# Optimization experiments

Hardware: AMD Instinct MI355X
Metric: run time of the kernel (lower is better)

The kernel has to match this reference:

```python
import jax, jax.numpy as jnp
import numpy as np

N_NODES = 50000
N_FEAT = 63          # nodeChannels C = N_FEAT + 1 = 64
N_EDGES = 800000
N_LABELS = 10000
BATCH = 4
N_LAYERS = 5
C = N_FEAT + 1


def setup_inputs() -> dict:
    key = jax.random.key(0)
    ks = jax.random.split(key, 16)
    s = 0.05  # small init scale for numerical sanity
    return {
        "cov": jax.random.normal(ks[0], (BATCH, N_LABELS), jnp.float32),
        "nodes": jax.random.normal(ks[1], (N_NODES, N_FEAT), jnp.float32),
        "edges": jax.random.randint(ks[2], (2, N_EDGES), 0, N_NODES, jnp.int64 if jax.config.jax_enable_x64 else jnp.int32),
        "count2label": jnp.arange(N_LABELS, dtype=jnp.int32),
        "ggc_weight": jax.random.normal(ks[3], (N_LAYERS, C, C), jnp.float32) * s,
        "gru_w_ih": jax.random.normal(ks[4], (3 * C, C), jnp.float32) * s,
        "gru_w_hh": jax.random.normal(ks[5], (3 * C, C), jnp.float32) * s,
        "gru_b_ih": jax.random.normal(ks[6], (3 * C,), jnp.float32) * s,
        "gru_b_hh": jax.random.normal(ks[7], (3 * C,), jnp.float32) * s,
        "ai_w": jax.random.normal(ks[8], (2 * C, 2 * C), jnp.float32) * s,
        "ai_b": jax.random.normal(ks[9], (2 * C,), jnp.float32) * s,
        "aj_w": jax.random.normal(ks[10], (2 * C, 2 * C), jnp.float32) * s,
        "aj_b": jax.random.normal(ks[11], (2 * C,), jnp.float32) * s,
        "mlp_w": jax.random.normal(ks[12], (256, 2 * C), jnp.float32) * s,
        "mlp_b": jax.random.normal(ks[13], (256,), jnp.float32) * s,
        "critic_w": jax.random.normal(ks[14], (1, 256), jnp.float32) * s,
        "critic_b": jax.random.normal(ks[15], (1,), jnp.float32) * s,
    }


def _gru_cell(m, h, w_ih, w_hh, b_ih, b_hh):
    # torch GRUCell, gate order r, z, n
    gx = m @ w_ih.T + b_ih   # [..., 3C]
    gh = h @ w_hh.T + b_hh
    c = h.shape[-1]
    xr, xz, xn = gx[..., :c], gx[..., c:2 * c], gx[..., 2 * c:]
    hr, hz, hn = gh[..., :c], gh[..., c:2 * c], gh[..., 2 * c:]
    r = jax.nn.sigmoid(xr + hr)
    z = jax.nn.sigmoid(xz + hz)
    n = jnp.tanh(xn + r * hn)
    return (1.0 - z) * n + z * h


def reference(cov, nodes, edges, count2label, ggc_weight,
              gru_w_ih, gru_w_hh, gru_b_ih, gru_b_hh,
              ai_w, ai_b, aj_w, aj_b, mlp_w, mlp_b, critic_w, critic_b):
    n, f = nodes.shape
    b = cov.shape[0]
    # scatter coverage into per-graph node channel: covInGraph[count2label] = cov
    cov_in_graph = jnp.zeros((b, n), cov.dtype).at[:, count2label].set(cov)
    # batched node input [B, N, C]; batched graph = B identical copies w/ offset edges
    x0 = jnp.concatenate(
        [jnp.broadcast_to(nodes, (b, n, f)), cov_in_graph[..., None]], axis=-1)
    src, dst = edges[0], edges[1]

    def scatter_add(mb):  # [N, C] -> [N, C]: sum messages from source at target
        return jax.ops.segment_sum(mb[src], dst, num_segments=n)

    x = x0
    for i in range(ggc_weight.shape[0]):
        m = x @ ggc_weight[i]                     # dense per-layer matmul [B,N,C]
        agg = jax.vmap(scatter_add)(m)            # edge scatter-add propagate
        x = _gru_cell(agg, x, gru_w_ih, gru_w_hh, gru_b_ih, gru_b_hh)

    # attention gate: sigmoid(Wi cat) * relu(Wj cat), cat = [x, x0]
    cat = jnp.concatenate([x, x0], axis=-1)       # [B, N, 2C]
    att = jax.nn.sigmoid(cat @ ai_w.T + ai_b) * jax.nn.relu(cat @ aj_w.T + aj_b)
    pooled = jax.nn.relu(att.sum(axis=1))         # global_add_pool -> [B, 2C]
    state = jax.nn.relu(pooled @ mlp_w.T + mlp_b) # graphmlp
    return state @ critic_w.T + critic_b          # critic value [B, 1]
```

## Files before the change

### kernel.cpp

```cpp
#include <hip/hip_runtime.h>
#include <math.h>

#define NN 50000
#define NF 63
#define NE 800000
#define NL 10000
#define NB 4
#define NLAY 5
#define BN (NB*NN)
#define NTILES (BN/64)
#define SCAN_NBLK ((NN+255)/256)
#define HIST_NBLK ((NE+255)/256)
#define X0_NBLK ((BN*16)/256)
#define COV_NBLK ((NB*NL+255)/256)

using f32x4  = __attribute__((ext_vector_type(4))) float;
using f32x2  = __attribute__((ext_vector_type(2))) float;
using bf16x8 = __attribute__((ext_vector_type(8))) __bf16;

__device__ __forceinline__ float frcp(float x){ return __builtin_amdgcn_rcpf(x); }
__device__ __forceinline__ float sigm(float v){ return frcp(1.f + __expf(-v)); }
__device__ __forceinline__ float tanh_f(float v){ return fmaf(-2.f, frcp(__expf(2.f*v) + 1.f), 1.f); }

__device__ __forceinline__ ushort f2bf(float f){
    uint u = __builtin_bit_cast(uint, f);
    u += 0x7fffu + ((u >> 16) & 1u);
    return (ushort)(u >> 16);
}
__device__ __forceinline__ float bf_lo(uint v){ return __builtin_bit_cast(float, v << 16); }
__device__ __forceinline__ float bfu(ushort v){ return __builtin_bit_cast(float, ((uint)v) << 16); }

__device__ __forceinline__ uchar f2fp8(float v){
    int enc = __builtin_amdgcn_cvt_pk_fp8_f32(v, v, 0, false);
    return (uchar)(enc & 0xff);
}

__device__ __forceinline__ bf16x8 ldfrag(const ushort* p){
    uint4 v = *(const uint4*)p;
    return __builtin_bit_cast(bf16x8, v);
}
__device__ __forceinline__ f32x4 MFMA(bf16x8 a, bf16x8 b, f32x4 c){
    return __builtin_amdgcn_mfma_f32_16x16x32_bf16(a, b, c, 0, 0, 0);
}

__global__ void k_setup(const int* __restrict__ edges, int* __restrict__ cnt,
                        const float* __restrict__ wih, const float* __restrict__ whh,
                        const float* __restrict__ aiw, const float* __restrict__ ajw,
                        const float* __restrict__ ggc,
                        ushort* __restrict__ whhb, ushort* __restrict__ aiwb,
                        ushort* __restrict__ ajwb, ushort* __restrict__ wfb,
                        const float* __restrict__ nodes, ushort* __restrict__ x0I,
                        uchar* __restrict__ x0F){
    int bid = blockIdx.x;
    if (bid < HIST_NBLK){
        int e = bid*256 + threadIdx.x;
        if (e < NE) atomicAdd(&cnt[edges[NE + e]], 1);
        return;
    }
    if (bid < HIST_NBLK + 416){
        int i = (bid - HIST_NBLK)*256 + threadIdx.x;
        if (i < 12288)        whhb[i]        = f2bf(whh[i]);
        else if (i < 28672)   aiwb[i-12288]  = f2bf(aiw[i-12288]);
        else if (i < 45056)   ajwb[i-28672]  = f2bf(ajw[i-28672]);
        else if (i < 106496){
            int t = i - 45056;
            int lay = t / 12288;
            int rem = t % 12288;
            int n = rem >> 6, k = rem & 63;
            const float* W  = ggc + lay*4096 + k*64;
            const float* wr = wih + n*64;
            float s = 0.f;
            #pragma unroll 8
            for (int c = 0; c < 64; ++c) s = fmaf(W[c], wr[c], s);
            wfb[t] = f2bf(s);
        }
        return;
    }
    int f = (bid - HIST_NBLK - 416)*256 + threadIdx.x;
    int row = f >> 4, c4 = f & 15;
    int n = row % NN, b = row / NN;
    float v[4];
    #pragma unroll
    for (int i = 0; i < 4; ++i){
        int c = c4*4 + i;
        v[i] = (c < NF) ? nodes[(size_t)n*NF + c] : 0.f;
    }
    uint2 pk;
    pk.x = (uint)f2bf(v[0]) | ((uint)f2bf(v[1]) << 16);
    pk.y = (uint)f2bf(v[2]) | ((uint)f2bf(v[3]) << 16);
    *(uint2*)(x0I + ((size_t)n*4 + b)*64 + c4*4) = pk;
    if (b == 0){
        uint q = 0;
        q = (uint)__builtin_amdgcn_cvt_pk_fp8_f32(v[0], v[1], (int)q, false);
        q = (uint)__builtin_amdgcn_cvt_pk_fp8_f32(v[2], v[3], (int)q, true);
        *(uint*)(x0F + (size_t)n*64 + c4*4) = q;
    }
}

__global__ void k_scan1(const int* __restrict__ cnt, int* __restrict__ tmp, int* __restrict__ bsum,
                        const float* __restrict__ cov, const int* __restrict__ c2l,
                        ushort* __restrict__ x0I, ushort* __restrict__ covB){
    if (blockIdx.x >= SCAN_NBLK){
        int i = (blockIdx.x - SCAN_NBLK)*256 + threadIdx.x;
        if (i < NB*NL){
            int b = i / NL, j = i % NL;
            int nd = c2l[j];
            ushort vb = f2bf(cov[i]);
            x0I[((size_t)nd*4 + b)*64 + 63] = vb;
            covB[(size_t)nd*4 + b] = vb;
        }
        return;
    }
    __shared__ int sh[256];
    int tx = threadIdx.x, i = blockIdx.x*256 + tx;
    int v = (i < NN) ? cnt[i] : 0;
    sh[tx] = v; __syncthreads();
    for (int off = 1; off < 256; off <<= 1){
        int u = (tx >= off) ? sh[tx-off] : 0;
        __syncthreads();
        sh[tx] += u;
        __syncthreads();
    }
    int incl = sh[tx];
    if (i < NN) tmp[i] = incl - v;
    if (tx == 255) bsum[blockIdx.x] = incl;
}

__global__ void k_scan3(const int* __restrict__ tmp, const int* __restrict__ bsum,
                        int* __restrict__ row_start, int* __restrict__ cursor){
    __shared__ int sh[256];
    int tx = threadIdx.x;
    int v = (tx < SCAN_NBLK) ? bsum[tx] : 0;
    sh[tx] = v; __syncthreads();
    for (int off = 1; off < 256; off <<= 1){
        int u = (tx >= off) ? sh[tx-off] : 0;
        __syncthreads();
        sh[tx] += u;
        __syncthreads();
    }
    int boff = sh[blockIdx.x] - bsum[blockIdx.x];
    int i = blockIdx.x*256 + tx;
    if (i < NN){
        int rs = tmp[i] + boff;
        row_start[i] = rs;
        cursor[i] = rs;
    }
    if (i == 0) row_start[NN] = NE;
}

__global__ void k_fillcsr(const int* __restrict__ edges, int* __restrict__ cursor, int* __restrict__ csr_src){
    int e = blockIdx.x*256 + threadIdx.x;
    if (e < NE){
        int d = edges[NE + e];
        int pos = atomicAdd(&cursor[d], 1);
        csr_src[pos] = edges[e];
    }
}

__device__ __forceinline__ void gather0q(const uchar* __restrict__ x0F,
                                         const ushort* __restrict__ covB,
                                         const int* __restrict__ csr_src,
                                         int e0, int e1, int l,
                                         ushort* __restrict__ sAgg, int rbase){
    const int qn = l >> 4, t = l & 15;
    const uint off = (uint)(t*4);
    f32x2 a01 = (f32x2){0.f,0.f}, a23 = (f32x2){0.f,0.f};
    float c = 0.f;
    int e = e0;
    for (; e + 16 <= e1; e += 16){
        int s[16];
        #pragma unroll
        for (int j = 0; j < 16; ++j) s[j] = csr_src[e + j];
        uint v[16];
        #pragma unroll
        for (int j = 0; j < 16; ++j) v[j] = *(const uint*)(x0F + (size_t)s[j]*64 + off);
        #pragma unroll
        for (int j = 0; j < 16; ++j){
            a01 += __builtin_amdgcn_cvt_pk_f32_fp8(v[j], false);
            a23 += __builtin_amdgcn_cvt_pk_f32_fp8(v[j], true);
        }
        if (t < 4){
            #pragma unroll
            for (int j = 0; j < 16; ++j) c += bf_lo((uint)covB[(size_t)s[j]*4 + t]);
        }
    }
    if (e < e1){
        int s[16];
        #pragma unroll
        for (int j = 0; j < 16; ++j){ int ee = e + j; if (ee >= e1) ee = e1 - 1; s[j] = csr_src[ee]; }
        uint v[16];
        #pragma unroll
        for (int j = 0; j < 16; ++j){
            v[j] = *(const uint*)(x0F + (size_t)s[j]*64 + off);
            if (e + j >= e1) v[j] = 0u;
        }
        #pragma unroll
        for (int j = 0; j < 16; ++j){
            a01 += __builtin_amdgcn_cvt_pk_f32_fp8(v[j], false);
            a23 += __builtin_amdgcn_cvt_pk_f32_fp8(v[j], true);
        }
        if (t < 4){
            #pragma unroll
            for (int j = 0; j < 16; ++j){
                float cv = bf_lo((uint)covB[(size_t)s[j]*4 + t]);
                c += (e + j < e1) ? cv : 0.f;
            }
        }
    }
    uint2 pk;
    pk.x = (uint)f2bf(a01.x) | ((uint)f2bf(a01.y) << 16);
    pk.y = (uint)f2bf(a23.x) | ((uint)f2bf(a23.y) << 16);
    #pragma unroll
    for (int b = 0; b < 4; ++b){
        float cb = __shfl(c, (l & 48) | b);
        uint2 o = pk;
        if (t == 15) o.y = (o.y & 0xffffu) | ((uint)f2bf(cb) << 16);
        *(uint2*)(&sAgg[(size_t)(rbase + qn*4 + b)*72 + t*4]) = o;
    }
}

__device__ __forceinline__ void load8(uint4 v[8], const uchar* __restrict__ xF,
                                      const int* __restrict__ csr_src,
                                      int eb, int e1, uint off){
    #pragma unroll
    for (int j = 0; j < 8; ++j){
        int ee = eb + j; if (ee >= e1) ee = e1 - 1;
        int s = csr_src[ee];
        v[j] = *(const uint4*)(xF + (size_t)s*256 + off);
    }
}
__device__ __forceinline__ void conv8(const uint4 v[8], int eb, int e1, f32x2 ac[8]){
    #pragma unroll
    for (int j = 0; j < 8; ++j){
        uint4 x = v[j];
        if (eb + j >= e1) x = (uint4){0u,0u,0u,0u};
        ac[0] += __builtin_amdgcn_cvt_pk_f32_fp8(x.x, false);
        ac[1] += __builtin_amdgcn_cvt_pk_f32_fp8(x.x, true);
        ac[2] += __builtin_amdgcn_cvt_pk_f32_fp8(x.y, false);
        ac[3] += __builtin_amdgcn_cvt_pk_f32_fp8(x.y, true);
        ac[4] += __builtin_amdgcn_cvt_pk_f32_fp8(x.z, false);
        ac[5] += __builtin_amdgcn_cvt_pk_f32_fp8(x.z, true);
        ac[6] += __builtin_amdgcn_cvt_pk_f32_fp8(x.w, false);
        ac[7] += __builtin_amdgcn_cvt_pk_f32_fp8(x.w, true);
    }
}

__device__ __forceinline__ void gather4q(const uchar* __restrict__ xF,
                                         const int* __restrict__ csr_src,
                                         int e0, int e1, int l,
                                         ushort* __restrict__ sAgg, int rbase){
    const int qn = l >> 4;
    const int t  = l & 15;
    const uint off = (uint)(t*16);
    f32x2 ac[8];
    #pragma unroll
    for (int k = 0; k < 8; ++k) ac[k] = (f32x2){0.f,0.f};

    uint4 va[8], vb[8];
    int eb = e0;
    if (eb < e1){
        load8(va, xF, csr_src, eb, e1, off);
        while (true){
            int ebB = eb + 8;
            if (ebB >= e1){ conv8(va, eb, e1, ac); break; }
            load8(vb, xF, csr_src, ebB, e1, off);
            conv8(va, eb, e1, ac);
            int ebA = ebB + 8;
            if (ebA >= e1){ conv8(vb, ebB, e1, ac); break; }
            load8(va, xF, csr_src, ebA, e1, off);
            conv8(vb, ebB, e1, ac);
            eb = ebA;
        }
    }

    const int row = rbase + qn*4 + (t >> 2);
    const int c0  = (t & 3)*16;
    uint4 o0, o1;
    o0.x = (uint)f2bf(ac[0].x) | ((uint)f2bf(ac[0].y) << 16);
    o0.y = (uint)f2bf(ac[1].x) | ((uint)f2bf(ac[1].y) << 16);
    o0.z = (uint)f2bf(ac[2].x) | ((uint)f2bf(ac[2].y) << 16);
    o0.w = (uint)f2bf(ac[3].x) | ((uint)f2bf(ac[3].y) << 16);
    o1.x = (uint)f2bf(ac[4].x) | ((uint)f2bf(ac[4].y) << 16);
    o1.y = (uint)f2bf(ac[5].x) | ((uint)f2bf(ac[5].y) << 16);
    o1.z = (uint)f2bf(ac[6].x) | ((uint)f2bf(ac[6].y) << 16);
    o1.w = (uint)f2bf(ac[7].x) | ((uint)f2bf(ac[7].y) << 16);
    *(uint4*)(&sAgg[(size_t)row*72 + c0])     = o0;
    *(uint4*)(&sAgg[(size_t)row*72 + c0 + 8]) = o1;
}

__device__ __forceinline__ void gru_core(const ushort* sAgg, const ushort* sX,
                                         const ushort* __restrict__ wfb, const ushort* __restrict__ whhb,
                                         const float* __restrict__ bih, const float* __restrict__ bhh,
                                         int li, int q, int n0, float xv[4][4]){
    f32x4 Cr[4], Cz[4], Cxn[4], Chn[4];
    #pragma unroll
    for (int m = 0; m < 4; ++m){
        Cr[m]=(f32x4){0.f,0.f,0.f,0.f}; Cz[m]=(f32x4){0.f,0.f,0.f,0.f};
        Cxn[m]=(f32x4){0.f,0.f,0.f,0.f}; Chn[m]=(f32x4){0.f,0.f,0.f,0.f};
    }
    __builtin_amdgcn_s_setprio(1);
    #pragma unroll
    for (int ks = 0; ks < 4; ++ks){
        const ushort* wb = (ks < 2) ? wfb : whhb;
        const ushort* sT = (ks < 2) ? sAgg : sX;
        const int kb = (ks & 1)*32;
        bf16x8 Br = ldfrag(wb + (size_t)(n0 + li)*64 + kb + q*8);
        bf16x8 Bz = ldfrag(wb + (size_t)(64 + n0 + li)*64 + kb + q*8);
        bf16x8 Bn = ldfrag(wb + (size_t)(128 + n0 + li)*64 + kb + q*8);
        #pragma unroll
        for (int m = 0; m < 4; ++m){
            bf16x8 A = ldfrag(&sT[(m*16 + li)*72 + kb + q*8]);
            Cr[m] = MFMA(A, Br, Cr[m]);
            Cz[m] = MFMA(A, Bz, Cz[m]);
            if (ks < 2) Cxn[m] = MFMA(A, Bn, Cxn[m]);
            else        Chn[m] = MFMA(A, Bn, Chn[m]);
        }
    }
    __builtin_amdgcn_s_setprio(0);
    const int c = n0 + li;
    const float br_ = bih[c]     + bhh[c];
    const float bz_ = bih[64+c]  + bhh[64+c];
    const float bn_ = bih[128+c];
    const float bh_ = bhh[128+c];
    #pragma unroll
    for (int m = 0; m < 4; ++m){
        #pragma unroll
        for (int rg = 0; rg < 4; ++rg){
            int rl = m*16 + q*4 + rg;
            float r = sigm(Cr[m][rg] + br_);
            float z = sigm(Cz[m][rg] + bz_);
            float nng = tanh_f(Cxn[m][rg] + bn_ + r*(Chn[m][rg] + bh_));
            xv[m][rg] = (1.f - z)*nng + z*bfu(sX[rl*72 + c]);
        }
    }
}

__device__ __forceinline__ void store_state(ushort* sAgg, uchar* sF8, int tx, int w, int li, int q,
                                            const float xv[4][4], int R0,
                                            ushort* __restrict__ xout, uchar* __restrict__ xFout){
    __syncthreads();
    const int c = 16*w + li;
    #pragma unroll
    for (int m = 0; m < 4; ++m)
        #pragma unroll
        for (int rg = 0; rg < 4; ++rg){
            int r = m*16 + q*4 + rg;
            sAgg[r*72 + c] = f2bf(xv[m][rg]);
            sF8[r*64 + c]  = f2fp8(xv[m][rg]);
        }
    __syncthreads();
    #pragma unroll
    for (int it = 0; it < 2; ++it){
        int idx = it*256 + tx, r = idx >> 3, g = idx & 7;
        *(uint4*)(xout + (size_t)(R0 + r)*64 + g*8) = *(const uint4*)(&sAgg[r*72 + g*8]);
    }
    {
        int r = tx >> 2, g = tx & 3;
        *(uint4*)(xFout + (size_t)(R0 + r)*64 + g*16) = *(const uint4*)(&sF8[r*64 + g*16]);
    }
}

__global__ __launch_bounds__(256, 4) void k_gru0f(const uchar* __restrict__ x0F,
                                               const ushort* __restrict__ covB,
                                               const int* __restrict__ row_start,
                                               const int* __restrict__ csr_src,
                                               const ushort* __restrict__ x0I,
                                               const ushort* __restrict__ wfb, const ushort* __restrict__ whhb,
                                               const float* __restrict__ bih, const float* __restrict__ bhh,
                                               ushort* __restrict__ xout, uchar* __restrict__ xFout){
    __shared__ __align__(16) ushort sAgg[64*72];
    __shared__ __align__(16) ushort sX[64*72];
    __shared__ __align__(16) uchar  sF8[64*64];
    const int tx = threadIdx.x;
    const int l  = tx & 63, li = l & 15, q = l >> 4;
    const int w  = __builtin_amdgcn_readfirstlane(tx >> 6);
    const int R0 = blockIdx.x*64;
    const int d  = blockIdx.x*16 + w*4 + (l >> 4);
    const int e0 = row_start[d], e1 = row_start[d+1];

    #pragma unroll
    for (int it = 0; it < 2; ++it){
        int idx = it*256 + tx, r = idx >> 3, g = idx & 7;
        *(uint4*)(&sX[r*72 + g*8]) = *(const uint4*)(x0I + (size_t)(R0 + r)*64 + g*8);
    }
    gather0q(x0F, covB, csr_src, e0, e1, l, sAgg, w*16);
    __syncthreads();

    float xv[4][4];
    gru_core(sAgg, sX, wfb, whhb, bih, bhh, li, q, 16*w, xv);
    store_state(sAgg, sF8, tx, w, li, q, xv, R0, xout, xFout);
}

__global__ __launch_bounds__(256, 4) void k_gruFf(const uchar* __restrict__ xFin,
                                               const int* __restrict__ row_start,
                                               const int* __restrict__ csr_src,
                                               const ushort* __restrict__ xsrc,
                                               const ushort* __restrict__ wfb, const ushort* __restrict__ whhb,
                                               const float* __restrict__ bih, const float* __restrict__ bhh,
                                               ushort* __restrict__ xout, uchar* __restrict__ xFout){
    __shared__ __align__(16) ushort sAgg[64*72];
    __shared__ __align__(16) ushort sX[64*72];
    __shared__ __align__(16) uchar  sF8[64*64];
    const int tx = threadIdx.x;
    const int l  = tx & 63, li = l & 15, q = l >> 4;
    const int w  = __builtin_amdgcn_readfirstlane(tx >> 6);
    const int R0 = blockIdx.x*64;
    const int d  = blockIdx.x*16 + w*4 + (l >> 4);
    const int e0 = row_start[d], e1 = row_start[d+1];

    #pragma unroll
    for (int it = 0; it < 2; ++it){
        int idx = it*256 + tx, r = idx >> 3, g = idx & 7;
        *(uint4*)(&sX[r*72 + g*8]) = *(const uint4*)(xsrc + (size_t)(R0 + r)*64 + g*8);
    }
    gather4q(xFin, csr_src, e0, e1, l, sAgg, w*16);
    __syncthreads();

    float xv[4][4];
    gru_core(sAgg, sX, wfb, whhb, bih, bhh, li, q, 16*w, xv);
    store_state(sAgg, sF8, tx, w, li, q, xv, R0, xout, xFout);
}

__global__ __launch_bounds__(256, 4) void k_gruLf(const uchar* __restrict__ xFin,
                                               const int* __restrict__ row_start,
                                               const int* __restrict__ csr_src,
                                               const ushort* __restrict__ xsrc,
                                               const ushort* __restrict__ wfb, const ushort* __restrict__ whhb,
                                               const float* __restrict__ bih, const float* __restrict__ bhh,
                                               const ushort* __restrict__ x0I,
                                               const ushort* __restrict__ aiwb, const float* __restrict__ aib,
                                               const ushort* __restrict__ ajwb, const float* __restrict__ ajb,
                                               float* __restrict__ pooled16){
    __shared__ __align__(16) ushort sAgg[64*72];
    __shared__ __align__(16) ushort sX[64*72];
    const int tx = threadIdx.x;
    const int l  = tx & 63, li = l & 15, q = l >> 4;
    const int w  = __builtin_amdgcn_readfirstlane(tx >> 6);
    const int R0 = blockIdx.x*64;
    const int d  = blockIdx.x*16 + w*4 + (l >> 4);
    const int e0 = row_start[d], e1 = row_start[d+1];

    #pragma unroll
    for (int it = 0; it < 2; ++it){
        int idx = it*256 + tx, r = idx >> 3, g = idx & 7;
        *(uint4*)(&sX[r*72 + g*8]) = *(const uint4*)(xsrc + (size_t)(R0 + r)*64 + g*8);
    }
    gather4q(xFin, csr_src, e0, e1, l, sAgg, w*16);
    __syncthreads();

    float xv[4][4];
    gru_core(sAgg, sX, wfb, whhb, bih, bhh, li, q, 16*w, xv);
    __syncthreads();

    const int c = 16*w + li;
    #pragma unroll
    for (int m = 0; m < 4; ++m)
        #pragma unroll
        for (int rg = 0; rg < 4; ++rg)
            sAgg[(m*16 + q*4 + rg)*72 + c] = f2bf(xv[m][rg]);
    #pragma unroll
    for (int it = 0; it < 2; ++it){
        int idx = it*256 + tx, r = idx >> 3, g = idx & 7;
        *(uint4*)(&sX[r*72 + g*8]) = *(const uint4*)(x0I + (size_t)(R0 + r)*64 + g*8);
    }
    __syncthreads();

    f32x4 Ai[2][4], Aj[2][4];
    #pragma unroll
    for (int t = 0; t < 2; ++t)
        #pragma unroll
        for (int m = 0; m < 4; ++m){ Ai[t][m]=(f32x4){0.f,0.f,0.f,0.f}; Aj[t][m]=(f32x4){0.f,0.f,0.f,0.f}; }

    const int nb0 = 32*w;
    __builtin_amdgcn_s_setprio(1);
    #pragma unroll
    for (int ks = 0; ks < 4; ++ks){
        const ushort* sT = (ks < 2) ? sAgg : sX;
        const int kb = (ks & 1)*32;
        bf16x8 Bi[2], Bj[2];
        #pragma unroll
        for (int t = 0; t < 2; ++t){
            Bi[t] = ldfrag(aiwb + (size_t)(nb0 + 16*t + li)*128 + ks*32 + q*8);
            Bj[t] = ldfrag(ajwb + (size_t)(nb0 + 16*t + li)*128 + ks*32 + q*8);
        }
        #pragma unroll
        for (int m = 0; m < 4; ++m){
            bf16x8 A = ldfrag(&sT[(m*16 + li)*72 + kb + q*8]);
            #pragma unroll
            for (int t = 0; t < 2; ++t){
                Ai[t][m] = MFMA(A, Bi[t], Ai[t][m]);
                Aj[t][m] = MFMA(A, Bj[t], Aj[t][m]);
            }
        }
    }
    __builtin_amdgcn_s_setprio(0);

    float* pb = pooled16 + (size_t)(blockIdx.x & 15)*512;
    #pragma unroll
    for (int t = 0; t < 2; ++t){
        int cc = nb0 + 16*t + li;
        float bia = aib[cc], bja = ajb[cc];
        float vs[4] = {0.f, 0.f, 0.f, 0.f};
        #pragma unroll
        for (int m = 0; m < 4; ++m){
            #pragma unroll
            for (int rg = 0; rg < 4; ++rg){
                float s = sigm(Ai[t][m][rg] + bia);
                float a = Aj[t][m][rg] + bja;
                a = a > 0.f ? a : 0.f;
                vs[rg] += s*a;
            }
        }
        #pragma unroll
        for (int b = 0; b < 4; ++b){
            vs[b] += __shfl_xor(vs[b], 16);
            vs[b] += __shfl_xor(vs[b], 32);
        }
        if (l < 16){
            #pragma unroll
            for (int b = 0; b < 4; ++b) atomicAdd(&pb[b*128 + nb0 + 16*t + l], vs[b]);
        }
    }
}

__global__ void k_final(const float* __restrict__ pooled16, const float* __restrict__ mw,
                        const float* __restrict__ mb, const float* __restrict__ cw,
                        const float* __restrict__ cb, float* __restrict__ out){
    __shared__ float red[256];
    int t = threadIdx.x;
    int b = blockIdx.x;
    float acc = mb[t];
    #pragma unroll 4
    for (int k = 0; k < 128; ++k){
        float p = 0.f;
        #pragma unroll
        for (int kb = 0; kb < 16; ++kb) p += pooled16[kb*512 + b*128 + k];
        p = p > 0.f ? p : 0.f;
        acc = fmaf(p, mw[t*128 + k], acc);
    }
    float st = acc > 0.f ? acc : 0.f;
    red[t] = st * cw[t];
    __syncthreads();
    for (int off = 128; off > 0; off >>= 1){
        if (t < off) red[t] += red[t + off];
        __syncthreads();
    }
    if (t == 0) out[b] = red[0] + cb[0];
}

extern "C" void kernel_launch(void* const* d_in, const int* in_sizes, int n_in,
                              void* d_out, int out_size, void* d_ws, size_t ws_size,
                              hipStream_t stream) {
    const float* cov   = (const float*)d_in[0];
    const float* nodes = (const float*)d_in[1];
    const int*   edges = (const int*)d_in[2];
    const int*   c2l   = (const int*)d_in[3];
    const float* ggc   = (const float*)d_in[4];
    const float* wih   = (const float*)d_in[5];
    const float* whh   = (const float*)d_in[6];
    const float* bih   = (const float*)d_in[7];
    const float* bhh   = (const float*)d_in[8];
    const float* aiw   = (const float*)d_in[9];
    const float* aib   = (const float*)d_in[10];
    const float* ajw   = (const float*)d_in[11];
    const float* ajb   = (const float*)d_in[12];
    const float* mlpw  = (const float*)d_in[13];
    const float* mlpb  = (const float*)d_in[14];
    const float* cw    = (const float*)d_in[15];
    const float* cb    = (const float*)d_in[16];
    float* out = (float*)d_out;

    const size_t XSZ = (size_t)BN * 64;
    float* ws = (float*)d_ws;
    float* pooled16 = ws;
    ushort* xS    = (ushort*)(pooled16 + 8192);
    ushort* x0I   = xS + XSZ;
    ushort* aggx  = x0I + XSZ;
    ushort* covB  = aggx + XSZ;
    ushort* whhb  = covB + (size_t)NN*4;
    ushort* aiwb  = whhb + 12288;
    ushort* ajwb  = aiwb + 16384;
    ushort* wfb   = ajwb + 16384;
    uchar* xF     = (uchar*)(wfb + 61440);
    uchar* x0F    = xF + XSZ;
    int* cnt       = (int*)(x0F + (size_t)NN*64);
    int* tmp       = cnt + NN;
    int* bsum      = tmp + NN;
    int* boff      = bsum + 256;
    int* row_start = boff + 256;
    int* cursor    = row_start + (NN + 1);
    int* csr_src   = cursor + NN;

    hipMemsetAsync(cnt, 0, (size_t)NN*sizeof(int), stream);
    hipMemsetAsync(pooled16, 0, 8192*sizeof(float), stream);
    hipMemsetAsync(covB, 0, (size_t)NN*4*sizeof(ushort), stream);

    k_setup<<<HIST_NBLK + 416 + X0_NBLK, 256, 0, stream>>>(edges, cnt, wih, whh, aiw, ajw, ggc,
                                                           whhb, aiwb, ajwb, wfb,
                                                           nodes, x0I, x0F);
    k_scan1<<<SCAN_NBLK + COV_NBLK, 256, 0, stream>>>(cnt, tmp, bsum, cov, c2l, x0I, covB);
    k_scan3<<<SCAN_NBLK, 256, 0, stream>>>(tmp, bsum, row_start, cursor);
    k_fillcsr<<<(NE + 255)/256, 256, 0, stream>>>(edges, cursor, csr_src);

    uchar* xFbuf[2] = { xF, (uchar*)aggx };

    for (int i = 0; i < NLAY; ++i){
        const ushort* wf = wfb + (size_t)i*12288;
        if (i == 0){
            k_gru0f<<<NTILES, 256, 0, stream>>>(x0F, covB, row_start, csr_src, x0I,
                                                wf, whhb, bih, bhh, xS, xFbuf[0]);
        } else if (i < NLAY - 1){
            k_gruFf<<<NTILES, 256, 0, stream>>>(xFbuf[(i+1)&1], row_start, csr_src, xS,
                                                wf, whhb, bih, bhh, xS, xFbuf[i&1]);
        } else {
            k_gruLf<<<NTILES, 256, 0, stream>>>(xFbuf[(i+1)&1], row_start, csr_src, xS,
                                                wf, whhb, bih, bhh,
                                                x0I, aiwb, aib, ajwb, ajb, pooled16);
        }
    }

    k_final<<<NB, 256, 0, stream>>>(pooled16, mlpw, mlpb, cw, cb, out);
    (void)in_sizes; (void)n_in; (void)out_size; (void)ws_size;
}
```

Measured before the change: 505.8 us.

## Halve rows per block and split each node's edge gather across two half-warps

Each block now handles 32 rows (8 graph nodes x 4 batches) instead of 64. Each node's neighbor list is split between two 16-lane halves that process interleaved chunks of 8 edges and then combine their partial sums with a cross-lane shuffle. Launch bounds are raised to 8 blocks per CU and the grid doubles. The goal is more memory-level parallelism and occupancy for the latency-bound gather. In exchange, the per-block GRU matmul tiles shrink, so the weight fragments are reloaded more often per row and MFMA reuse drops.

```diff
diff --git a/kernel.cpp b/kernel.cpp
--- a/kernel.cpp
+++ b/kernel.cpp
@@ -8,7 +8,9 @@
 #define NB 4
 #define NLAY 5
 #define BN (NB*NN)
-#define NTILES (BN/64)
+#define RPB 32
+#define NPB 8
+#define NT2 (BN/RPB)
 #define SCAN_NBLK ((NN+255)/256)
 #define HIST_NBLK ((NE+255)/256)
 #define X0_NBLK ((BN*16)/256)
@@ -161,61 +163,49 @@
                                          const ushort* __restrict__ covB,
                                          const int* __restrict__ csr_src,
                                          int e0, int e1, int l,
-                                         ushort* __restrict__ sAgg, int rbase){
-    const int qn = l >> 4, t = l & 15;
+                                         ushort* __restrict__ sAgg, int nodeRow){
+    const int h = (l >> 4) & 1;
+    const int t = l & 15;
     const uint off = (uint)(t*4);
     f32x2 a01 = (f32x2){0.f,0.f}, a23 = (f32x2){0.f,0.f};
     float c = 0.f;
-    int e = e0;
-    for (; e + 16 <= e1; e += 16){
-        int s[16];
-        #pragma unroll
-        for (int j = 0; j < 16; ++j) s[j] = csr_src[e + j];
-        uint v[16];
-        #pragma unroll
-        for (int j = 0; j < 16; ++j) v[j] = *(const uint*)(x0F + (size_t)s[j]*64 + off);
-        #pragma unroll
-        for (int j = 0; j < 16; ++j){
+    for (int eb = e0 + 8*h; eb < e1; eb += 16){
+        int s[8];
+        #pragma unroll
+        for (int j = 0; j < 8; ++j){ int ee = eb + j; if (ee >= e1) ee = e1 - 1; s[j] = csr_src[ee]; }
+        uint v[8];
+        #pragma unroll
+        for (int j = 0; j < 8; ++j){
+            v[j] = *(const uint*)(x0F + (size_t)s[j]*64 + off);
+            if (eb + j >= e1) v[j] = 0u;
+        }
+        #pragma unroll
+        for (int j = 0; j < 8; ++j){
             a01 += __builtin_amdgcn_cvt_pk_f32_fp8(v[j], false);
             a23 += __builtin_amdgcn_cvt_pk_f32_fp8(v[j], true);
         }
         if (t < 4){
             #pragma unroll
-            for (int j = 0; j < 16; ++j) c += bf_lo((uint)covB[(size_t)s[j]*4 + t]);
-        }
-    }
-    if (e < e1){
-        int s[16];
-        #pragma unroll
-        for (int j = 0; j < 16; ++j){ int ee = e + j; if (ee >= e1) ee = e1 - 1; s[j] = csr_src[ee]; }
-        uint v[16];
-        #pragma unroll
-        for (int j = 0; j < 16; ++j){
-            v[j] = *(const uint*)(x0F + (size_t)s[j]*64 + off);
-            if (e + j >= e1) v[j] = 0u;
-        }
-        #pragma unroll
-        for (int j = 0; j < 16; ++j){
-            a01 += __builtin_amdgcn_cvt_pk_f32_fp8(v[j], false);
-            a23 += __builtin_amdgcn_cvt_pk_f32_fp8(v[j], true);
-        }
-        if (t < 4){
-            #pragma unroll
-            for (int j = 0; j < 16; ++j){
+            for (int j = 0; j < 8; ++j){
                 float cv = bf_lo((uint)covB[(size_t)s[j]*4 + t]);
-                c += (e + j < e1) ? cv : 0.f;
+                c += (eb + j < e1) ? cv : 0.f;
             }
         }
     }
-    uint2 pk;
-    pk.x = (uint)f2bf(a01.x) | ((uint)f2bf(a01.y) << 16);
-    pk.y = (uint)f2bf(a23.x) | ((uint)f2bf(a23.y) << 16);
-    #pragma unroll
-    for (int b = 0; b < 4; ++b){
-        float cb = __shfl(c, (l & 48) | b);
-        uint2 o = pk;
-        if (t == 15) o.y = (o.y & 0xffffu) | ((uint)f2bf(cb) << 16);
-        *(uint2*)(&sAgg[(size_t)(rbase + qn*4 + b)*72 + t*4]) = o;
+    a01.x += __shfl_xor(a01.x, 16); a01.y += __shfl_xor(a01.y, 16);
+    a23.x += __shfl_xor(a23.x, 16); a23.y += __shfl_xor(a23.y, 16);
+    c     += __shfl_xor(c, 16);
+    if (h == 0){
+        uint2 pk;
+        pk.x = (uint)f2bf(a01.x) | ((uint)f2bf(a01.y) << 16);
+        pk.y = (uint)f2bf(a23.x) | ((uint)f2bf(a23.y) << 16);
+        #pragma unroll
+        for (int b = 0; b < 4; ++b){
+            float cb = __shfl(c, (l & 48) | b);
+            uint2 o = pk;
+            if (t == 15) o.y = (o.y & 0xffffu) | ((uint)f2bf(cb) << 16);
+            *(uint2*)(&sAgg[(size_t)(nodeRow + b)*72 + t*4]) = o;
+        }
     }
 }
 
@@ -248,53 +238,59 @@
 __device__ __forceinline__ void gather4q(const uchar* __restrict__ xF,
                                          const int* __restrict__ csr_src,
                                          int e0, int e1, int l,
-                                         ushort* __restrict__ sAgg, int rbase){
-    const int qn = l >> 4;
-    const int t  = l & 15;
+                                         ushort* __restrict__ sAgg, int nodeRow){
+    const int h = (l >> 4) & 1;
+    const int t = l & 15;
     const uint off = (uint)(t*16);
     f32x2 ac[8];
     #pragma unroll
     for (int k = 0; k < 8; ++k) ac[k] = (f32x2){0.f,0.f};
 
     uint4 va[8], vb[8];
-    int eb = e0;
+    int eb = e0 + 8*h;
     if (eb < e1){
         load8(va, xF, csr_src, eb, e1, off);
         while (true){
-            int ebB = eb + 8;
+            int ebB = eb + 16;
             if (ebB >= e1){ conv8(va, eb, e1, ac); break; }
             load8(vb, xF, csr_src, ebB, e1, off);
             conv8(va, eb, e1, ac);
-            int ebA = ebB + 8;
+            int ebA = ebB + 16;
             if (ebA >= e1){ conv8(vb, ebB, e1, ac); break; }
             load8(va, xF, csr_src, ebA, e1, off);
             conv8(vb, ebB, e1, ac);
             eb = ebA;
         }
     }
-
-    const int row = rbase + qn*4 + (t >> 2);
-    const int c0  = (t & 3)*16;
-    uint4 o0, o1;
-    o0.x = (uint)f2bf(ac[0].x) | ((uint)f2bf(ac[0].y) << 16);
-    o0.y = (uint)f2bf(ac[1].x) | ((uint)f2bf(ac[1].y) << 16);
-    o0.z = (uint)f2bf(ac[2].x) | ((uint)f2bf(ac[2].y) << 16);
-    o0.w = (uint)f2bf(ac[3].x) | ((uint)f2bf(ac[3].y) << 16);
-    o1.x = (uint)f2bf(ac[4].x) | ((uint)f2bf(ac[4].y) << 16);
-    o1.y = (uint)f2bf(ac[5].x) | ((uint)f2bf(ac[5].y) << 16);
-    o1.z = (uint)f2bf(ac[6].x) | ((uint)f2bf(ac[6].y) << 16);
-    o1.w = (uint)f2bf(ac[7].x) | ((uint)f2bf(ac[7].y) << 16);
-    *(uint4*)(&sAgg[(size_t)row*72 + c0])     = o0;
-    *(uint4*)(&sAgg[(size_t)row*72 + c0 + 8]) = o1;
+    #pragma unroll
+    for (int k = 0; k < 8; ++k){
+        ac[k].x += __shfl_xor(ac[k].x, 16);
+        ac[k].y += __shfl_xor(ac[k].y, 16);
+    }
+    if (h == 0){
+        const int row = nodeRow + (t >> 2);
+        const int c0  = (t & 3)*16;
+        uint4 o0, o1;
+        o0.x = (uint)f2bf(ac[0].x) | ((uint)f2bf(ac[0].y) << 16);
+        o0.y = (uint)f2bf(ac[1].x) | ((uint)f2bf(ac[1].y) << 16);
+        o0.z = (uint)f2bf(ac[2].x) | ((uint)f2bf(ac[2].y) << 16);
+        o0.w = (uint)f2bf(ac[3].x) | ((uint)f2bf(ac[3].y) << 16);
+        o1.x = (uint)f2bf(ac[4].x) | ((uint)f2bf(ac[4].y) << 16);
+        o1.y = (uint)f2bf(ac[5].x) | ((uint)f2bf(ac[5].y) << 16);
+        o1.z = (uint)f2bf(ac[6].x) | ((uint)f2bf(ac[6].y) << 16);
+        o1.w = (uint)f2bf(ac[7].x) | ((uint)f2bf(ac[7].y) << 16);
+        *(uint4*)(&sAgg[(size_t)row*72 + c0])     = o0;
+        *(uint4*)(&sAgg[(size_t)row*72 + c0 + 8]) = o1;
+    }
 }
 
 __device__ __forceinline__ void gru_core(const ushort* sAgg, const ushort* sX,
                                          const ushort* __restrict__ wfb, const ushort* __restrict__ whhb,
                                          const float* __restrict__ bih, const float* __restrict__ bhh,
-                                         int li, int q, int n0, float xv[4][4]){
-    f32x4 Cr[4], Cz[4], Cxn[4], Chn[4];
-    #pragma unroll
-    for (int m = 0; m < 4; ++m){
+                                         int li, int q, int n0, float xv[2][4]){
+    f32x4 Cr[2], Cz[2], Cxn[2], Chn[2];
+    #pragma unroll
+    for (int m = 0; m < 2; ++m){
         Cr[m]=(f32x4){0.f,0.f,0.f,0.f}; Cz[m]=(f32x4){0.f,0.f,0.f,0.f};
         Cxn[m]=(f32x4){0.f,0.f,0.f,0.f}; Chn[m]=(f32x4){0.f,0.f,0.f,0.f};
     }
@@ -308,7 +304,7 @@
         bf16x8 Bz = ldfrag(wb + (size_t)(64 + n0 + li)*64 + kb + q*8);
         bf16x8 Bn = ldfrag(wb + (size_t)(128 + n0 + li)*64 + kb + q*8);
         #pragma unroll
-        for (int m = 0; m < 4; ++m){
+        for (int m = 0; m < 2; ++m){
             bf16x8 A = ldfrag(&sT[(m*16 + li)*72 + kb + q*8]);
             Cr[m] = MFMA(A, Br, Cr[m]);
             Cz[m] = MFMA(A, Bz, Cz[m]);
@@ -323,7 +319,7 @@
     const float bn_ = bih[128+c];
     const float bh_ = bhh[128+c];
     #pragma unroll
-    for (int m = 0; m < 4; ++m){
+    for (int m = 0; m < 2; ++m){
         #pragma unroll
         for (int rg = 0; rg < 4; ++rg){
             int rl = m*16 + q*4 + rg;
@@ -336,12 +332,12 @@
 }
 
 __device__ __forceinline__ void store_state(ushort* sAgg, uchar* sF8, int tx, int w, int li, int q,
-                                            const float xv[4][4], int R0,
+                                            const float xv[2][4], int R0,
                                             ushort* __restrict__ xout, uchar* __restrict__ xFout){
     __syncthreads();
     const int c = 16*w + li;
     #pragma unroll
-    for (int m = 0; m < 4; ++m)
+    for (int m = 0; m < 2; ++m)
         #pragma unroll
         for (int rg = 0; rg < 4; ++rg){
             int r = m*16 + q*4 + rg;
@@ -349,18 +345,17 @@
             sF8[r*64 + c]  = f2fp8(xv[m][rg]);
         }
     __syncthreads();
-    #pragma unroll
-    for (int it = 0; it < 2; ++it){
-        int idx = it*256 + tx, r = idx >> 3, g = idx & 7;
+    {
+        int r = tx >> 3, g = tx & 7;
         *(uint4*)(xout + (size_t)(R0 + r)*64 + g*8) = *(const uint4*)(&sAgg[r*72 + g*8]);
     }
-    {
+    if (tx < 128){
         int r = tx >> 2, g = tx & 3;
         *(uint4*)(xFout + (size_t)(R0 + r)*64 + g*16) = *(const uint4*)(&sF8[r*64 + g*16]);
     }
 }
 
-__global__ __launch_bounds__(256, 4) void k_gru0f(const uchar* __restrict__ x0F,
+__global__ __launch_bounds__(256, 8) void k_gru0f(const uchar* __restrict__ x0F,
                                                const ushort* __restrict__ covB,
                                                const int* __restrict__ row_start,
                                                const int* __restrict__ csr_src,
@@ -368,60 +363,60 @@
                                                const ushort* __restrict__ wfb, const ushort* __restrict__ whhb,
                                                const float* __restrict__ bih, const float* __restrict__ bhh,
                                                ushort* __restrict__ xout, uchar* __restrict__ xFout){
-    __shared__ __align__(16) ushort sAgg[64*72];
-    __shared__ __align__(16) ushort sX[64*72];
-    __shared__ __align__(16) uchar  sF8[64*64];
+    __shared__ __align__(16) ushort sAgg[RPB*72];
+    __shared__ __align__(16) ushort sX[RPB*72];
+    __shared__ __align__(16) uchar  sF8[RPB*64];
     const int tx = threadIdx.x;
     const int l  = tx & 63, li = l & 15, q = l >> 4;
     const int w  = __builtin_amdgcn_readfirstlane(tx >> 6);
-    const int R0 = blockIdx.x*64;
-    const int d  = blockIdx.x*16 + w*4 + (l >> 4);
+    const int R0 = blockIdx.x*RPB;
+    const int nd = tx >> 5;
+    const int d  = blockIdx.x*NPB + nd;
     const int e0 = row_start[d], e1 = row_start[d+1];
 
-    #pragma unroll
-    for (int it = 0; it < 2; ++it){
-        int idx = it*256 + tx, r = idx >> 3, g = idx & 7;
+    {
+        int r = tx >> 3, g = tx & 7;
         *(uint4*)(&sX[r*72 + g*8]) = *(const uint4*)(x0I + (size_t)(R0 + r)*64 + g*8);
     }
-    gather0q(x0F, covB, csr_src, e0, e1, l, sAgg, w*16);
-    __syncthreads();
-
-    float xv[4][4];
+    gather0q(x0F, covB, csr_src, e0, e1, l, sAgg, nd*4);
+    __syncthreads();
+
+    float xv[2][4];
     gru_core(sAgg, sX, wfb, whhb, bih, bhh, li, q, 16*w, xv);
     store_state(sAgg, sF8, tx, w, li, q, xv, R0, xout, xFout);
 }
 
-__global__ __launch_bounds__(256, 4) void k_gruFf(const uchar* __restrict__ xFin,
+__global__ __launch_bounds__(256, 8) void k_gruFf(const uchar* __restrict__ xFin,
                                                const int* __restrict__ row_start,
                                                const int* __restrict__ csr_src,
                                                const ushort* __restrict__ xsrc,
                                                const ushort* __restrict__ wfb, const ushort* __restrict__ whhb,
                                                const float* __restrict__ bih, const float* __restrict__ bhh,
                                                ushort* __restrict__ xout, uchar* __restrict__ xFout){
-    __shared__ __align__(16) ushort sAgg[64*72];
-    __shared__ __align__(16) ushort sX[64*72];
-    __shared__ __align__(16) uchar  sF8[64*64];
+    __shared__ __align__(16) ushort sAgg[RPB*72];
+    __shared__ __align__(16) ushort sX[RPB*72];
+    __shared__ __align__(16) uchar  sF8[RPB*64];
     const int tx = threadIdx.x;
     const int l  = tx & 63, li = l & 15, q = l >> 4;
     const int w  = __builtin_amdgcn_readfirstlane(tx >> 6);
-    const int R0 = blockIdx.x*64;
-    const int d  = blockIdx.x*16 + w*4 + (l >> 4);
+    const int R0 = blockIdx.x*RPB;
+    const int nd = tx >> 5;
+    const int d  = blockIdx.x*NPB + nd;
     const int e0 = row_start[d], e1 = row_start[d+1];
 
-    #pragma unroll
-    for (int it = 0; it < 2; ++it){
-        int idx = it*256 + tx, r = idx >> 3, g = idx & 7;
+    {
+        int r = tx >> 3, g = tx & 7;
         *(uint4*)(&sX[r*72 + g*8]) = *(const uint4*)(xsrc + (size_t)(R0 + r)*64 + g*8);
     }
-    gather4q(xFin, csr_src, e0, e1, l, sAgg, w*16);
-    __syncthreads();
-
-    float xv[4][4];
+    gather4q(xFin, csr_src, e0, e1, l, sAgg, nd*4);
+    __syncthreads();
+
+    float xv[2][4];
     gru_core(sAgg, sX, wfb, whhb, bih, bhh, li, q, 16*w, xv);
     store_state(sAgg, sF8, tx, w, li, q, xv, R0, xout, xFout);
 }
 
-__global__ __launch_bounds__(256, 4) void k_gruLf(const uchar* __restrict__ xFin,
+__global__ __launch_bounds__(256, 8) void k_gruLf(const uchar* __restrict__ xFin,
                                                const int* __restrict__ row_start,
                                                const int* __restrict__ csr_src,
                                                const ushort* __restrict__ xsrc,
@@ -431,45 +426,44 @@
                                                const ushort* __restrict__ aiwb, const float* __restrict__ aib,
                                                const ushort* __restrict__ ajwb, const float* __restrict__ ajb,
                                                float* __restrict__ pooled16){
-    __shared__ __align__(16) ushort sAgg[64*72];
-    __shared__ __align__(16) ushort sX[64*72];
+    __shared__ __align__(16) ushort sAgg[RPB*72];
+    __shared__ __align__(16) ushort sX[RPB*72];
     const int tx = threadIdx.x;
     const int l  = tx & 63, li = l & 15, q = l >> 4;
     const int w  = __builtin_amdgcn_readfirstlane(tx >> 6);
-    const int R0 = blockIdx.x*64;
-    const int d  = blockIdx.x*16 + w*4 + (l >> 4);
+    const int R0 = blockIdx.x*RPB;
+    const int nd = tx >> 5;
+    const int d  = blockIdx.x*NPB + nd;
     const int e0 = row_start[d], e1 = row_start[d+1];
 
-    #pragma unroll
-    for (int it = 0; it < 2; ++it){
-        int idx = it*256 + tx, r = idx >> 3, g = idx & 7;
+    {
+        int r = tx >> 3, g = tx & 7;
         *(uint4*)(&sX[r*72 + g*8]) = *(const uint4*)(xsrc + (size_t)(R0 + r)*64 + g*8);
     }
-    gather4q(xFin, csr_src, e0, e1, l, sAgg, w*16);
-    __syncthreads();
-
-    float xv[4][4];
+    gather4q(xFin, csr_src, e0, e1, l, sAgg, nd*4);
+    __syncthreads();
+
+    float xv[2][4];
     gru_core(sAgg, sX, wfb, whhb, bih, bhh, li, q, 16*w, xv);
     __syncthreads();
 
     const int c = 16*w + li;
     #pragma unroll
-    for (int m = 0; m < 4; ++m)
+    for (int m = 0; m < 2; ++m)
         #pragma unroll
         for (int rg = 0; rg < 4; ++rg)
             sAgg[(m*16 + q*4 + rg)*72 + c] = f2bf(xv[m][rg]);
-    #pragma unroll
-    for (int it = 0; it < 2; ++it){
-        int idx = it*256 + tx, r = idx >> 3, g = idx & 7;
+    {
+        int r = tx >> 3, g = tx & 7;
         *(uint4*)(&sX[r*72 + g*8]) = *(const uint4*)(x0I + (size_t)(R0 + r)*64 + g*8);
     }
     __syncthreads();
 
-    f32x4 Ai[2][4], Aj[2][4];
+    f32x4 Ai[2][2], Aj[2][2];
     #pragma unroll
     for (int t = 0; t < 2; ++t)
         #pragma unroll
-        for (int m = 0; m < 4; ++m){ Ai[t][m]=(f32x4){0.f,0.f,0.f,0.f}; Aj[t][m]=(f32x4){0.f,0.f,0.f,0.f}; }
+        for (int m = 0; m < 2; ++m){ Ai[t][m]=(f32x4){0.f,0.f,0.f,0.f}; Aj[t][m]=(f32x4){0.f,0.f,0.f,0.f}; }
 
     const int nb0 = 32*w;
     __builtin_amdgcn_s_setprio(1);
@@ -484,7 +478,7 @@
             Bj[t] = ldfrag(ajwb + (size_t)(nb0 + 16*t + li)*128 + ks*32 + q*8);
         }
         #pragma unroll
-        for (int m = 0; m < 4; ++m){
+        for (int m = 0; m < 2; ++m){
             bf16x8 A = ldfrag(&sT[(m*16 + li)*72 + kb + q*8]);
             #pragma unroll
             for (int t = 0; t < 2; ++t){
@@ -502,7 +496,7 @@
         float bia = aib[cc], bja = ajb[cc];
         float vs[4] = {0.f, 0.f, 0.f, 0.f};
         #pragma unroll
-        for (int m = 0; m < 4; ++m){
+        for (int m = 0; m < 2; ++m){
             #pragma unroll
             for (int rg = 0; rg < 4; ++rg){
                 float s = sigm(Ai[t][m][rg] + bia);
@@ -607,15 +601,15 @@
     for (int i = 0; i < NLAY; ++i){
         const ushort* wf = wfb + (size_t)i*12288;
         if (i == 0){
-            k_gru0f<<<NTILES, 256, 0, stream>>>(x0F, covB, row_start, csr_src, x0I,
-                                                wf, whhb, bih, bhh, xS, xFbuf[0]);
+            k_gru0f<<<NT2, 256, 0, stream>>>(x0F, covB, row_start, csr_src, x0I,
+                                             wf, whhb, bih, bhh, xS, xFbuf[0]);
         } else if (i < NLAY - 1){
-            k_gruFf<<<NTILES, 256, 0, stream>>>(xFbuf[(i+1)&1], row_start, csr_src, xS,
-                                                wf, whhb, bih, bhh, xS, xFbuf[i&1]);
+            k_gruFf<<<NT2, 256, 0, stream>>>(xFbuf[(i+1)&1], row_start, csr_src, xS,
+                                             wf, whhb, bih, bhh, xS, xFbuf[i&1]);
         } else {
-            k_gruLf<<<NTILES, 256, 0, stream>>>(xFbuf[(i+1)&1], row_start, csr_src, xS,
-                                                wf, whhb, bih, bhh,
-                                                x0I, aiwb, aib, ajwb, ajb, pooled16);
+            k_gruLf<<<NT2, 256, 0, stream>>>(xFbuf[(i+1)&1], row_start, csr_src, xS,
+                                             wf, whhb, bih, bhh,
+                                             x0I, aiwb, aib, ajwb, ajb, pooled16);
         }
     }
 
```

Result: slower. 972.9 us (+92.4%).
